# Optimization experiments

Measured on AMD Instinct MI355X. Metric: run time of the kernel, lower is better.

Reference implementation:

```python
import jax, jax.numpy as jnp
import numpy as np

# Config matching init_kwargs: dim=256, input_resolution=(64,64), num_heads=8,
# stride=2, dynamic_factor=2, window_size=8, Attention_Group=2, postype='rel', k=None
DIM, H, W = 256, 64, 64
HEADS, HG, STRIDE, WS, FACTOR = 8, 2, 2, 8, 2.0
GC = DIM // HG                 # channels per attention group (offset net width)
HC = DIM // HEADS              # per-head channels
RH, RW = H // STRIDE, W // STRIDE
WH, WW = H // WS, W // WS
B = 2
MLP_HID = 4 * DIM
EPS = 1e-5


def _grid_sample(img, grid):
    # img: (N, C, H, W); grid: (N, Hg, Wg, 2) with (row, col) in [-1, 1].
    # Bilinear, align_corners=True, zero padding (matches F.grid_sample).
    N, C, Hi, Wi = img.shape
    rows = (grid[..., 0] + 1.0) * 0.5 * (Hi - 1)
    cols = (grid[..., 1] + 1.0) * 0.5 * (Wi - 1)
    r0f = jnp.floor(rows); c0f = jnp.floor(cols)
    wr = rows - r0f; wc = cols - c0f
    r0 = r0f.astype(jnp.int32); c0 = c0f.astype(jnp.int32)

    def gather(ri, ci):
        valid = ((ri >= 0) & (ri < Hi) & (ci >= 0) & (ci < Wi)).astype(img.dtype)
        rc = jnp.clip(ri, 0, Hi - 1); cc = jnp.clip(ci, 0, Wi - 1)
        vals = jax.vmap(lambda im, r, c: im[:, r, c])(img, rc, cc)  # (N, C, Hg, Wg)
        return vals * valid[:, None]

    return (gather(r0, c0) * ((1 - wr) * (1 - wc))[:, None]
            + gather(r0, c0 + 1) * ((1 - wr) * wc)[:, None]
            + gather(r0 + 1, c0) * (wr * (1 - wc))[:, None]
            + gather(r0 + 1, c0 + 1) * (wr * wc)[:, None])


def _ln2d(z, g, b):
    mu = jnp.mean(z, axis=1, keepdims=True)
    var = jnp.var(z, axis=1, keepdims=True)
    return (z - mu) * jax.lax.rsqrt(var + EPS) * g[None, :, None, None] + b[None, :, None, None]


def _conv1x1(z, w, b=None):
    out = jnp.einsum('oc,bchw->bohw', w, z)
    return out if b is None else out + b[None, :, None, None]


def _forward(x, ln1_g, ln1_b, q_w, q_b, k_w, k_b, v_w, v_b,
             off1_w, off2_w, off3_w, bn_g, bn_b, bn_m, bn_v, off4_w,
             posembed, proj_w, proj_b, ln2_g, ln2_b,
             mlp_w1, mlp_b1, mlp_w2, mlp_b2):
    Bx, C = x.shape[0], x.shape[1]
    R, NW, WT = RH * RW, WH * WW, WS * WS
    scale = C ** -0.5  # original uses dim**-0.5 (not head_dim) as default qk scale

    xa = _ln2d(x, ln1_g, ln1_b)
    q = _conv1x1(xa, q_w, q_b)

    # ---- per-group offset prediction: 3 depthwise strided convs -> BN -> GELU -> 1x1 ----
    qg = q.reshape(Bx * HG, GC, H, W)

    def dw(z, w):
        return jax.lax.conv_general_dilated(z, w, (2, 2), ((1, 1), (1, 1)),
                feature_group_count=GC, dimension_numbers=('NCHW', 'OIHW', 'NCHW'))

    o = dw(dw(dw(qg, off1_w), off2_w), off3_w)  # (B*HG, GC, WH, WW)
    o = (o - bn_m[None, :, None, None]) * jax.lax.rsqrt(bn_v + EPS)[None, :, None, None]
    o = o * bn_g[None, :, None, None] + bn_b[None, :, None, None]
    o = jax.nn.gelu(o, approximate=False)
    off = jnp.einsum('oc,bchw->bohw', off4_w, o)               # (B*HG, 2R, WH, WW)
    off = off.reshape(Bx * HG, 2, R, NW).transpose(0, 3, 2, 1)  # (B*HG, NW, R, 2)
    ranges = jnp.array([1.0 / H, 1.0 / W], dtype=x.dtype)
    off = jnp.tanh(off) * ranges * FACTOR

    # ---- reference points normalized to [-1, 1] (align_corners=True convention) ----
    ref_r = (jnp.arange(RH, dtype=x.dtype) * STRIDE) / (H - 1) * 2.0 - 1.0
    ref_c = (jnp.arange(RW, dtype=x.dtype) * STRIDE) / (W - 1) * 2.0 - 1.0
    ref = jnp.stack(jnp.meshgrid(ref_r, ref_c, indexing='ij'), axis=-1).reshape(R, 2)
    grid = off + ref[None, None]                                # (B*HG, NW, R, 2)

    # ---- deformable gather of values at predicted sample locations ----
    value = xa.reshape(Bx * HG, GC, H, W)
    samp = _grid_sample(value, grid).reshape(Bx, C, NW, R)

    kk = _conv1x1(samp, k_w, k_b).reshape(Bx * HEADS, HC, NW, R).transpose(0, 2, 1, 3)
    vv = _conv1x1(samp, v_w, v_b).reshape(Bx * HEADS, HC, NW, R).transpose(0, 2, 1, 3)

    # ---- windowed queries ----
    wq = q.reshape(Bx * HEADS, HC, H, W).transpose(0, 2, 3, 1)
    wq = wq.reshape(Bx * HEADS, WH, WS, WW, WS, HC).transpose(0, 1, 3, 2, 4, 5)
    wq = wq.reshape(Bx * HEADS, NW, WT, HC) * scale

    attn = jnp.einsum('nwqc,nwcr->nwqr', wq, kk)                # (B*h, NW, WT, R)

    # ---- relative position bias: query pixel vs. (stride-spaced) reference point ----
    rel_y = (jnp.arange(RH) * STRIDE)[None, :] - jnp.arange(H)[:, None] + (H - 1)  # (H, RH)
    rel_x = (jnp.arange(RW) * STRIDE)[None, :] - jnp.arange(W)[:, None] + (W - 1)  # (W, RW)
    t = posembed[:, rel_y, :]                                   # (h, H, RH, 2W-1)
    bias = t[:, :, :, rel_x]                                    # (h, H, RH, W, RW)
    bias = bias.transpose(0, 1, 3, 2, 4).reshape(HEADS, H, W, R)
    bias = bias.reshape(HEADS, WH, WS, WW, WS, R).transpose(0, 1, 3, 2, 4, 5)
    bias = bias.reshape(HEADS, NW, WT, R)

    attn = attn.reshape(Bx, HEADS, NW, WT, R) + bias[None]
    attn = jax.nn.softmax(attn, axis=-1).reshape(Bx * HEADS, NW, WT, R)
    out = jnp.einsum('nwqr,nwcr->nwqc', attn, vv)               # (B*h, NW, WT, HC)
    out = out.reshape(Bx * HEADS, WH, WW, WS, WS, HC).transpose(0, 1, 3, 2, 4, 5)
    out = out.reshape(Bx, HEADS, H, W, HC).transpose(0, 1, 4, 2, 3).reshape(Bx, C, H, W)
    out = _conv1x1(out, proj_w, proj_b)

    x = x + out
    xm = _ln2d(x, ln2_g, ln2_b)
    hdn = jax.nn.gelu(_conv1x1(xm, mlp_w1, mlp_b1), approximate=False)
    return x + _conv1x1(hdn, mlp_w2, mlp_b2)


def setup_inputs() -> dict:
    key = jax.random.key(0)
    ks = jax.random.split(key, 16)
    f32 = jnp.float32

    def n(k, shape, std=0.02):
        return jax.random.normal(k, shape, dtype=f32) * std

    R = RH * RW
    return {
        'x': jax.random.normal(ks[0], (B, DIM, H, W), dtype=f32),
        'ln1_g': jnp.ones((DIM,), f32), 'ln1_b': jnp.zeros((DIM,), f32),
        'q_w': n(ks[1], (DIM, DIM)), 'q_b': jnp.zeros((DIM,), f32),
        'k_w': n(ks[2], (DIM, DIM)), 'k_b': jnp.zeros((DIM,), f32),
        'v_w': n(ks[3], (DIM, DIM)), 'v_b': jnp.zeros((DIM,), f32),
        'off1_w': n(ks[4], (GC, 1, 3, 3)),
        'off2_w': n(ks[5], (GC, 1, 3, 3)),
        'off3_w': n(ks[6], (GC, 1, 3, 3)),
        'bn_g': jnp.ones((GC,), f32), 'bn_b': jnp.zeros((GC,), f32),
        'bn_m': jnp.zeros((GC,), f32), 'bn_v': jnp.ones((GC,), f32),
        'off4_w': n(ks[7], (2 * R, GC)),
        'posembed': n(ks[8], (HEADS, 2 * H - 1, 2 * W - 1), std=0.01),
        'proj_w': n(ks[9], (DIM, DIM)), 'proj_b': jnp.zeros((DIM,), f32),
        'ln2_g': jnp.ones((DIM,), f32), 'ln2_b': jnp.zeros((DIM,), f32),
        'mlp_w1': n(ks[10], (MLP_HID, DIM)), 'mlp_b1': jnp.zeros((MLP_HID,), f32),
        'mlp_w2': n(ks[11], (DIM, MLP_HID)), 'mlp_b2': jnp.zeros((DIM,), f32),
    }


def reference(x, ln1_g, ln1_b, q_w, q_b, k_w, k_b, v_w, v_b,
              off1_w, off2_w, off3_w, bn_g, bn_b, bn_m, bn_v, off4_w,
              posembed, proj_w, proj_b, ln2_g, ln2_b,
              mlp_w1, mlp_b1, mlp_w2, mlp_b2):
    return _forward(x, ln1_g, ln1_b, q_w, q_b, k_w, k_b, v_w, v_b,
                    off1_w, off2_w, off3_w, bn_g, bn_b, bn_m, bn_v, off4_w,
                    posembed, proj_w, proj_b, ln2_g, ln2_b,
                    mlp_w1, mlp_b1, mlp_w2, mlp_b2)
```

## Files before the change

### kernel.cpp

```cpp
#include <hip/hip_runtime.h>
#include <hip/hip_bf16.h>
#include <math.h>


typedef __hip_bfloat16 bf16;
typedef __bf16 bf16x8 __attribute__((ext_vector_type(8)));
typedef float f32x4 __attribute__((ext_vector_type(4)));

union U16x8 { uint4 u4; unsigned short us[8]; };

__device__ __forceinline__ float cvt(float x) { return x; }
__device__ __forceinline__ float cvt(bf16 x) { return __bfloat162float(x); }
__device__ __forceinline__ float b2f(unsigned short u) {
  union { float f; unsigned int v; } x; x.v = ((unsigned int)u) << 16; return x.f;
}
__device__ __forceinline__ unsigned short f2b(float f) {
  bf16 h = __float2bfloat16(f);
  return *reinterpret_cast<unsigned short*>(&h);
}
__device__ __forceinline__ float gelu_f(float x) {
  return 0.5f * x * (1.0f + erff(x * 0.7071067811865475f));
}
__device__ __forceinline__ void stout(float* p, float v) { *p = v; }
__device__ __forceinline__ void stout(bf16* p, float v) { *p = __float2bfloat16(v); }

__global__ __launch_bounds__(256) void ln1_kernel(
    const float* __restrict__ x, const float* __restrict__ g,
    const float* __restrict__ bta, bf16* __restrict__ out,
    float* __restrict__ xnhwc)
{
  __shared__ float s1[8][32], s2[8][32];
  __shared__ unsigned short tb[32][264];
  int t = threadIdx.x;
  int pos = t & 31, cs = t >> 5;
  int p = blockIdx.x * 32 + pos;
  int bb = p >> 12, hw = p & 4095;
  const float* xp = x + (size_t)bb * 256 * 4096 + hw;
  float vloc[32];
  float sum = 0.f, ss = 0.f;
#pragma unroll
  for (int i = 0; i < 32; ++i) {
    float v = xp[(size_t)(cs * 32 + i) * 4096];
    vloc[i] = v; sum += v; ss += v * v;
  }
  s1[cs][pos] = sum; s2[cs][pos] = ss;
  {
    float* xo = xnhwc + (size_t)p * 256 + cs * 32;
#pragma unroll
    for (int qd = 0; qd < 8; ++qd)
      *(float4*)(xo + qd * 4) = make_float4(vloc[qd*4], vloc[qd*4+1],
                                            vloc[qd*4+2], vloc[qd*4+3]);
  }
  __syncthreads();
  if (cs == 0) {
    float S = 0.f, Q = 0.f;
#pragma unroll
    for (int i = 0; i < 8; ++i) { S += s1[i][pos]; Q += s2[i][pos]; }
    float mu = S * (1.f / 256.f);
    float var = Q * (1.f / 256.f) - mu * mu;
    s1[0][pos] = mu;
    s2[0][pos] = rsqrtf(var + 1e-5f);
  }
  __syncthreads();
  float mu = s1[0][pos], rs = s2[0][pos];
#pragma unroll
  for (int i = 0; i < 32; ++i) {
    int c = cs * 32 + i;
    tb[pos][c] = f2b((vloc[i] - mu) * rs * g[c] + bta[c]);
  }
  __syncthreads();
  int px = t >> 3, grp = t & 7;
  bf16* op = out + ((size_t)blockIdx.x * 32 + px) * 256 + grp * 32;
#pragma unroll
  for (int q = 0; q < 4; ++q)
    *(uint4*)(op + q * 8) = *(const uint4*)&tb[px][grp * 32 + q * 8];
}

__global__ __launch_bounds__(256) void ln2_kernel(
    const bf16* __restrict__ xin, const float* __restrict__ g,
    const float* __restrict__ bta, bf16* __restrict__ out)
{
  __shared__ float sa[8][32], sb[8][32];
  __shared__ float mu_s[32], rs_s[32];
  int t = threadIdx.x;
  int px = t >> 3, grp = t & 7;
  size_t p = (size_t)blockIdx.x * 32 + px;
  const bf16* xp = xin + p * 256 + grp * 32;
  float v[32]; float sum = 0.f, ss = 0.f;
#pragma unroll
  for (int q = 0; q < 4; ++q) {
    U16x8 u; u.u4 = *(const uint4*)(xp + q * 8);
#pragma unroll
    for (int j = 0; j < 8; ++j) {
      float f = b2f(u.us[j]); v[q * 8 + j] = f; sum += f; ss += f * f;
    }
  }
  sa[grp][px] = sum; sb[grp][px] = ss;
  __syncthreads();
  if (t < 32) {
    float S = 0.f, Q = 0.f;
#pragma unroll
    for (int i = 0; i < 8; ++i) { S += sa[i][t]; Q += sb[i][t]; }
    float mu = S * (1.f / 256.f);
    mu_s[t] = mu;
    rs_s[t] = rsqrtf(Q * (1.f / 256.f) - mu * mu + 1e-5f);
  }
  __syncthreads();
  float mu = mu_s[px], rs = rs_s[px];
  bf16* op = out + p * 256 + grp * 32;
#pragma unroll
  for (int q = 0; q < 4; ++q) {
    U16x8 o;
#pragma unroll
    for (int j = 0; j < 8; ++j) {
      int c = grp * 32 + q * 8 + j;
      o.us[j] = f2b((v[q * 8 + j] - mu) * rs * g[c] + bta[c]);
    }
    *(uint4*)(op + q * 8) = o.u4;
  }
}

template<int OUTM, int RESM, int ACT>
__global__ __launch_bounds__(256) void mgemm_kernel(
    const bf16* __restrict__ A, const float* __restrict__ Bw,
    const float* __restrict__ bias, const void* __restrict__ res,
    void* __restrict__ out, int N, int K, int lda, int ldb)
{
  constexpr int AB_BYTES = (128 * 72 + 64 * 72) * 2;
  constexpr int T_BYTES  = 64 * 133 * 4;
  constexpr int SH_BYTES = (OUTM == 1 && T_BYTES > AB_BYTES) ? T_BYTES : AB_BYTES;
  __shared__ __attribute__((aligned(16))) char shraw[SH_BYTES];
  auto As = reinterpret_cast<unsigned short(*)[72]>(shraw);
  auto Bs = reinterpret_cast<unsigned short(*)[72]>(shraw + 128 * 72 * 2);
  float (*T)[133] = reinterpret_cast<float(*)[133]>(shraw);

  int t = threadIdx.x;
  int m0 = blockIdx.y * 128, n0 = blockIdx.x * 64;
  int lane = t & 63, w = t >> 6;
  int l15 = lane & 15, quad = lane >> 4;
  int wm = (w >> 1) * 64, wn = (w & 1) * 32;
  f32x4 acc[4][2];
#pragma unroll
  for (int mt = 0; mt < 4; ++mt)
#pragma unroll
    for (int nt = 0; nt < 2; ++nt) acc[mt][nt] = (f32x4){0.f, 0.f, 0.f, 0.f};

  for (int k0 = 0; k0 < K; k0 += 64) {
#pragma unroll
    for (int i = 0; i < 4; ++i) {
      int idx = t + i * 256;
      int m = idx >> 3, oc = (idx & 7) * 8;
      *(uint4*)&As[m][oc] = *(const uint4*)(A + (size_t)(m0 + m) * lda + k0 + oc);
    }
    {
      int n = t >> 2, h = (t & 3) * 16;
      const float* bp = Bw + (size_t)(n0 + n) * ldb + k0 + h;
      float4 f0 = *(const float4*)(bp);
      float4 f1 = *(const float4*)(bp + 4);
      float4 f2 = *(const float4*)(bp + 8);
      float4 f3 = *(const float4*)(bp + 12);
      U16x8 u0, u1;
      u0.us[0] = f2b(f0.x); u0.us[1] = f2b(f0.y); u0.us[2] = f2b(f0.z); u0.us[3] = f2b(f0.w);
      u0.us[4] = f2b(f1.x); u0.us[5] = f2b(f1.y); u0.us[6] = f2b(f1.z); u0.us[7] = f2b(f1.w);
      u1.us[0] = f2b(f2.x); u1.us[1] = f2b(f2.y); u1.us[2] = f2b(f2.z); u1.us[3] = f2b(f2.w);
      u1.us[4] = f2b(f3.x); u1.us[5] = f2b(f3.y); u1.us[6] = f2b(f3.z); u1.us[7] = f2b(f3.w);
      *(uint4*)&Bs[n][h] = u0.u4;
      *(uint4*)&Bs[n][h + 8] = u1.u4;
    }
    __syncthreads();
#pragma unroll
    for (int ks = 0; ks < 2; ++ks) {
      bf16x8 af[4], bfr[2];
#pragma unroll
      for (int mt = 0; mt < 4; ++mt)
        af[mt] = __builtin_bit_cast(bf16x8,
            *(const uint4*)&As[wm + mt * 16 + l15][ks * 32 + quad * 8]);
#pragma unroll
      for (int nt = 0; nt < 2; ++nt)
        bfr[nt] = __builtin_bit_cast(bf16x8,
            *(const uint4*)&Bs[wn + nt * 16 + l15][ks * 32 + quad * 8]);
#pragma unroll
      for (int mt = 0; mt < 4; ++mt)
#pragma unroll
        for (int nt = 0; nt < 2; ++nt)
          acc[mt][nt] = __builtin_amdgcn_mfma_f32_16x16x32_bf16(
              af[mt], bfr[nt], acc[mt][nt], 0, 0, 0);
    }
    __syncthreads();
  }
  float bv[2];
#pragma unroll
  for (int nt = 0; nt < 2; ++nt)
    bv[nt] = bias ? bias[n0 + wn + nt * 16 + l15] : 0.f;
#pragma unroll
  for (int mt = 0; mt < 4; ++mt) {
#pragma unroll
    for (int nt = 0; nt < 2; ++nt) {
#pragma unroll
      for (int reg = 0; reg < 4; ++reg) {
        int m = m0 + wm + mt * 16 + quad * 4 + reg;
        int n = n0 + wn + nt * 16 + l15;
        float v = acc[mt][nt][reg] + bv[nt];
        if constexpr (ACT == 1) v = gelu_f(v);
        if constexpr (RESM == 1)
          v += ((const float*)res)[(size_t)m * N + n];
        if constexpr (RESM == 2)
          v += b2f(((const unsigned short*)res)[(size_t)m * N + n]);
        if constexpr (OUTM == 0)
          ((unsigned short*)out)[(size_t)m * N + n] = f2b(v);
        if constexpr (OUTM == 1)
          T[(n - n0)][(m - m0)] = v;
        if constexpr (OUTM == 3) {
          float val = tanhf(v) * (2.0f / 64.0f);
          int coord = n >> 10, r = n & 1023;
          int rc = coord ? (r & 31) : (r >> 5);
          float ref = rc * (4.0f / 63.0f) - 1.0f;
          float pix = (val + ref + 1.0f) * 31.5f;
          float* dst = coord ? (float*)res : (float*)out;
          dst[(size_t)m * 1024 + r] = pix;
        }
      }
    }
  }
  if constexpr (OUTM == 1) {
    __syncthreads();
    int nl = t >> 2, seg = t & 3;
    int bI = m0 >> 12, hw0 = m0 & 4095;
    float* op = (float*)out + ((size_t)bI * 256 + n0 + nl) * 4096 + hw0 + seg * 32;
#pragma unroll
    for (int k = 0; k < 32; ++k) op[k] = T[nl][seg * 32 + k];
  }
}

template<typename TI, typename TO, int IC>
__global__ __launch_bounds__(256) void dwconv_kernel(
    const TI* __restrict__ in, const float* __restrict__ wgt,
    TO* __restrict__ out, int Hi, int Wi, int Ho, int Wo, int fuse,
    const float* __restrict__ bg_, const float* __restrict__ bb_,
    const float* __restrict__ bm_, const float* __restrict__ bv_)
{
  int idx = blockIdx.x * 256 + threadIdx.x;
  int c = idx & 127;
  int pp = idx >> 7;
  int ow = pp % Wo, oh = (pp / Wo) % Ho, bgi = pp / (Wo * Ho);
  const TI* ip;
  if constexpr (IC == 256)
    ip = in + ((size_t)(bgi >> 1) * 4096) * 256 + (bgi & 1) * 128 + c;
  else
    ip = in + ((size_t)bgi * Hi * Wi) * 128 + c;
  float acc = 0.f;
#pragma unroll
  for (int ky = 0; ky < 3; ++ky) {
    int ih = oh * 2 - 1 + ky;
    if ((unsigned)ih >= (unsigned)Hi) continue;
#pragma unroll
    for (int kx = 0; kx < 3; ++kx) {
      int iw = ow * 2 - 1 + kx;
      if ((unsigned)iw >= (unsigned)Wi) continue;
      acc += wgt[c * 9 + ky * 3 + kx] * cvt(ip[(size_t)(ih * Wi + iw) * IC]);
    }
  }
  if (fuse) {
    acc = (acc - bm_[c]) * rsqrtf(bv_[c] + 1e-5f) * bg_[c] + bb_[c];
    acc = gelu_f(acc);
  }
  stout(out + idx, acc);
}

__device__ __forceinline__ void gather_issue(
    int rc0, int b, int nw, int gr_r, int choff,
    const float* __restrict__ rows_, const float* __restrict__ cols_,
    const unsigned short* __restrict__ Kimg, const unsigned short* __restrict__ Vimg,
    uint4* kc, uint4* vc, float* wgt)
{
#pragma unroll
  for (int g = 0; g < 2; ++g) {
    size_t cbase = ((size_t)(b * 2 + g) * 64 + nw) * 1024 + rc0 + gr_r;
    float rowf = rows_[cbase];
    float colf = cols_[cbase];
    float r0f = floorf(rowf), c0f = floorf(colf);
    float wr = rowf - r0f, wc = colf - c0f;
    int r0 = (int)r0f, c0 = (int)c0f;
    bool rv0 = ((unsigned)r0 < 64u), rv1 = ((unsigned)(r0 + 1) < 64u);
    bool cv0 = ((unsigned)c0 < 64u), cv1 = ((unsigned)(c0 + 1) < 64u);
    wgt[g * 4 + 0] = (rv0 && cv0) ? (1.f - wr) * (1.f - wc) : 0.f;
    wgt[g * 4 + 1] = (rv0 && cv1) ? (1.f - wr) * wc : 0.f;
    wgt[g * 4 + 2] = (rv1 && cv0) ? wr * (1.f - wc) : 0.f;
    wgt[g * 4 + 3] = (rv1 && cv1) ? wr * wc : 0.f;
    int ra = min(max(r0, 0), 63), rb2 = min(max(r0 + 1, 0), 63);
    int ca = min(max(c0, 0), 63), cb2 = min(max(c0 + 1, 0), 63);
    size_t pb = ((size_t)g * 8192 + (size_t)b * 4096) * 256 + choff;
    size_t o00 = pb + (size_t)(ra * 64 + ca) * 256;
    size_t o01 = pb + (size_t)(ra * 64 + cb2) * 256;
    size_t o10 = pb + (size_t)(rb2 * 64 + ca) * 256;
    size_t o11 = pb + (size_t)(rb2 * 64 + cb2) * 256;
    kc[g * 4 + 0] = *(const uint4*)(Kimg + o00); vc[g * 4 + 0] = *(const uint4*)(Vimg + o00);
    kc[g * 4 + 1] = *(const uint4*)(Kimg + o01); vc[g * 4 + 1] = *(const uint4*)(Vimg + o01);
    kc[g * 4 + 2] = *(const uint4*)(Kimg + o10); vc[g * 4 + 2] = *(const uint4*)(Vimg + o10);
    kc[g * 4 + 3] = *(const uint4*)(Kimg + o11); vc[g * 4 + 3] = *(const uint4*)(Vimg + o11);
  }
}

__global__ __launch_bounds__(256) void attn_kernel(
    const bf16* __restrict__ qbuf, const unsigned short* __restrict__ Kimg,
    const unsigned short* __restrict__ Vimg, const float* __restrict__ rows_,
    const float* __restrict__ cols_, const float* __restrict__ vbv,
    const float* __restrict__ pe, bf16* __restrict__ aout)
{
  __shared__ unsigned short ks[2][64][40];
  __shared__ unsigned short vs[2][32][80];
  __shared__ unsigned short PsQs[64][72];
  __shared__ unsigned short pesb[70][72];

  int blk = blockIdx.x;
  int b = blk & 1, head = (blk >> 1) & 7, nw = blk >> 4;
  int wh = nw >> 3, ww = nw & 7;
  int t = threadIdx.x;
  int lane = t & 63, w = t >> 6;
  int l15 = lane & 15, quad = lane >> 4;
  int qc0 = head * 32;
  int gr_r = t >> 2, gr_seg = t & 3;
  int choff = qc0 + gr_seg * 8;

  {
    int qt = t >> 2, oct = t & 3;
    int h = wh * 8 + (qt >> 3), wcol = ww * 8 + (qt & 7);
    const bf16* src = qbuf + ((size_t)b * 4096 + h * 64 + wcol) * 256 + qc0 + oct * 8;
    U16x8 u; u.u4 = *(const uint4*)src;
    U16x8 o;
#pragma unroll
    for (int j = 0; j < 8; ++j) o.us[j] = f2b(b2f(u.us[j]) * 0.0625f);
    *(uint4*)&PsQs[qt][oct * 8] = o.u4;
  }
  int ry0 = 56 - wh * 8, rx0 = 56 - ww * 8;
  for (int i = t; i < 70 * 70; i += 256) {
    int yy = i / 70, xx = i % 70;
    pesb[yy][xx] = f2b(pe[(size_t)head * 16129 + (ry0 + yy) * 127 + rx0 + xx]);
  }

  uint4 kc[8], vc[8];
  float wgt[8];
  gather_issue(0, b, nw, gr_r, choff, rows_, cols_, Kimg, Vimg, kc, vc, wgt);
  {
    float aK[8] = {0,0,0,0,0,0,0,0}, aV[8] = {0,0,0,0,0,0,0,0};
#pragma unroll
    for (int gc = 0; gc < 8; ++gc) {
      U16x8 ku, vu; ku.u4 = kc[gc]; vu.u4 = vc[gc];
      float wv = wgt[gc];
#pragma unroll
      for (int j = 0; j < 8; ++j) { aK[j] += wv * b2f(ku.us[j]); aV[j] += wv * b2f(vu.us[j]); }
    }
    U16x8 ok;
#pragma unroll
    for (int j = 0; j < 8; ++j) ok.us[j] = f2b(aK[j]);
    *(uint4*)&ks[0][gr_r][gr_seg * 8] = ok.u4;
#pragma unroll
    for (int j = 0; j < 8; ++j) vs[0][gr_seg * 8 + j][gr_r] = f2b(aV[j]);
  }
  __syncthreads();

  bf16x8 aQ;
  {
    uint4 u = *(const uint4*)&PsQs[w * 16 + l15][quad * 8];
    aQ = __builtin_bit_cast(bf16x8, u);
  }
  float m[4] = {-1e30f, -1e30f, -1e30f, -1e30f};
  float l[4] = {0.f, 0.f, 0.f, 0.f};
  f32x4 oacc[2];
  oacc[0] = (f32x4){0.f, 0.f, 0.f, 0.f};
  oacc[1] = (f32x4){0.f, 0.f, 0.f, 0.f};

  for (int c = 0; c < 16; ++c) {
    if (c) __syncthreads();
    int cur = c & 1, rc0 = c * 64;
    if (c < 15)
      gather_issue(rc0 + 64, b, nw, gr_r, choff, rows_, cols_, Kimg, Vimg, kc, vc, wgt);

    f32x4 s[4];
#pragma unroll
    for (int nt = 0; nt < 4; ++nt) {
      uint4 u = *(const uint4*)&ks[cur][nt * 16 + l15][quad * 8];
      bf16x8 bK = __builtin_bit_cast(bf16x8, u);
      f32x4 z = (f32x4){0.f, 0.f, 0.f, 0.f};
      s[nt] = __builtin_amdgcn_mfma_f32_16x16x32_bf16(aQ, bK, z, 0, 0, 0);
    }
#pragma unroll
    for (int nt = 0; nt < 4; ++nt) {
      int rg_ = nt * 16 + l15;
      int rrow = (rc0 + rg_) >> 5, rcol = rg_ & 31;
#pragma unroll
      for (int reg = 0; reg < 4; ++reg) {
        int q = w * 16 + quad * 4 + reg;
        s[nt][reg] += b2f(pesb[2 * rrow + 7 - (q >> 3)][2 * rcol + 7 - (q & 7)]);
      }
    }
    float alpha[4];
#pragma unroll
    for (int reg = 0; reg < 4; ++reg) {
      float mx = fmaxf(fmaxf(s[0][reg], s[1][reg]), fmaxf(s[2][reg], s[3][reg]));
      mx = fmaxf(mx, __shfl_xor(mx, 1, 64));
      mx = fmaxf(mx, __shfl_xor(mx, 2, 64));
      mx = fmaxf(mx, __shfl_xor(mx, 4, 64));
      mx = fmaxf(mx, __shfl_xor(mx, 8, 64));
      float mn = fmaxf(m[reg], mx);
      alpha[reg] = __expf(m[reg] - mn);
      m[reg] = mn;
      float ps = 0.f;
#pragma unroll
      for (int nt = 0; nt < 4; ++nt) {
        float p = __expf(s[nt][reg] - mn);
        PsQs[w * 16 + quad * 4 + reg][nt * 16 + l15] = f2b(p);
        ps += p;
      }
      ps += __shfl_xor(ps, 1, 64);
      ps += __shfl_xor(ps, 2, 64);
      ps += __shfl_xor(ps, 4, 64);
      ps += __shfl_xor(ps, 8, 64);
      l[reg] = l[reg] * alpha[reg] + ps;
      oacc[0][reg] *= alpha[reg];
      oacc[1][reg] *= alpha[reg];
    }
#pragma unroll
    for (int kst = 0; kst < 2; ++kst) {
      uint4 up = *(const uint4*)&PsQs[w * 16 + l15][kst * 32 + quad * 8];
      bf16x8 pA = __builtin_bit_cast(bf16x8, up);
#pragma unroll
      for (int nt2 = 0; nt2 < 2; ++nt2) {
        uint4 uv = *(const uint4*)&vs[cur][nt2 * 16 + l15][kst * 32 + quad * 8];
        bf16x8 vB = __builtin_bit_cast(bf16x8, uv);
        oacc[nt2] = __builtin_amdgcn_mfma_f32_16x16x32_bf16(pA, vB, oacc[nt2], 0, 0, 0);
      }
    }
    if (c < 15) {
      float aK[8] = {0,0,0,0,0,0,0,0}, aV[8] = {0,0,0,0,0,0,0,0};
#pragma unroll
      for (int gc = 0; gc < 8; ++gc) {
        U16x8 ku, vu; ku.u4 = kc[gc]; vu.u4 = vc[gc];
        float wv = wgt[gc];
#pragma unroll
        for (int j = 0; j < 8; ++j) { aK[j] += wv * b2f(ku.us[j]); aV[j] += wv * b2f(vu.us[j]); }
      }
      int nxt = cur ^ 1;
      U16x8 ok;
#pragma unroll
      for (int j = 0; j < 8; ++j) ok.us[j] = f2b(aK[j]);
      *(uint4*)&ks[nxt][gr_r][gr_seg * 8] = ok.u4;
#pragma unroll
      for (int j = 0; j < 8; ++j) vs[nxt][gr_seg * 8 + j][gr_r] = f2b(aV[j]);
    }
  }
#pragma unroll
  for (int nt2 = 0; nt2 < 2; ++nt2) {
    float vbias = vbv[qc0 + nt2 * 16 + l15];
#pragma unroll
    for (int reg = 0; reg < 4; ++reg) {
      int q = w * 16 + quad * 4 + reg;
      size_t p = (size_t)b * 4096 + (wh * 8 + (q >> 3)) * 64 + ww * 8 + (q & 7);
      aout[p * 256 + qc0 + nt2 * 16 + l15] =
          __float2bfloat16(oacc[nt2][reg] / l[reg] + vbias);
    }
  }
}

extern "C" void kernel_launch(void* const* d_in, const int* in_sizes, int n_in,
                              void* d_out, int out_size, void* d_ws, size_t ws_size,
                              hipStream_t stream) {
  (void)in_sizes; (void)n_in; (void)out_size; (void)ws_size;
  const float* x     = (const float*)d_in[0];
  const float* ln1g  = (const float*)d_in[1];
  const float* ln1b  = (const float*)d_in[2];
  const float* q_w   = (const float*)d_in[3];
  const float* q_b   = (const float*)d_in[4];
  const float* k_w   = (const float*)d_in[5];
  const float* k_b   = (const float*)d_in[6];
  const float* v_w   = (const float*)d_in[7];
  const float* v_b   = (const float*)d_in[8];
  const float* off1w = (const float*)d_in[9];
  const float* off2w = (const float*)d_in[10];
  const float* off3w = (const float*)d_in[11];
  const float* bng   = (const float*)d_in[12];
  const float* bnb   = (const float*)d_in[13];
  const float* bnm   = (const float*)d_in[14];
  const float* bnv   = (const float*)d_in[15];
  const float* off4w = (const float*)d_in[16];
  const float* pe    = (const float*)d_in[17];
  const float* pjw   = (const float*)d_in[18];
  const float* pjb   = (const float*)d_in[19];
  const float* ln2g  = (const float*)d_in[20];
  const float* ln2b  = (const float*)d_in[21];
  const float* w1    = (const float*)d_in[22];
  const float* b1    = (const float*)d_in[23];
  const float* w2    = (const float*)d_in[24];
  const float* b2    = (const float*)d_in[25];
  (void)k_b;
  float* outp = (float*)d_out;

  char* W = (char*)d_ws;
  bf16*  xa    = (bf16*) (W + 0);
  bf16*  qb    = (bf16*) (W + 4194304);
  float* dw1   = (float*)(W + 8388608);
  float* dw2   = (float*)(W + 10485760);
  bf16*  dw3b  = (bf16*) (W + 11010048);
  float* rows  = (float*)(W + 11141120);
  float* cols  = (float*)(W + 12189696);
  bf16*  Kimg  = (bf16*) (W + 13238272);
  bf16*  Vimg  = (bf16*) (W + 21626880);
  bf16*  x2    = (bf16*) (W + 30015488);
  float* xnhwc = (float*)(W + 34209792);
  bf16*  aout = xa;
  bf16*  xm   = qb;
  bf16*  hdn  = Kimg;

  ln1_kernel<<<256, 256, 0, stream>>>(x, ln1g, ln1b, xa, xnhwc);
  mgemm_kernel<0, 0, 0><<<dim3(4, 64), 256, 0, stream>>>(
      xa, q_w, q_b, nullptr, qb, 256, 256, 256, 256);
  dwconv_kernel<bf16, float, 256><<<2048, 256, 0, stream>>>(
      qb, off1w, dw1, 64, 64, 32, 32, 0, nullptr, nullptr, nullptr, nullptr);
  dwconv_kernel<float, float, 128><<<512, 256, 0, stream>>>(
      dw1, off2w, dw2, 32, 32, 16, 16, 0, nullptr, nullptr, nullptr, nullptr);
  dwconv_kernel<float, bf16, 128><<<128, 256, 0, stream>>>(
      dw2, off3w, dw3b, 16, 16, 8, 8, 1, bng, bnb, bnm, bnv);
  mgemm_kernel<3, 0, 0><<<dim3(32, 2), 256, 0, stream>>>(
      dw3b, off4w, nullptr, (const void*)cols, rows, 2048, 128, 128, 128);
  mgemm_kernel<0, 0, 0><<<dim3(4, 64), 256, 0, stream>>>(
      xa,       k_w,       nullptr, nullptr, Kimg,           256, 128, 256, 256);
  mgemm_kernel<0, 0, 0><<<dim3(4, 64), 256, 0, stream>>>(
      xa + 128, k_w + 128, nullptr, nullptr, Kimg + 2097152, 256, 128, 256, 256);
  mgemm_kernel<0, 0, 0><<<dim3(4, 64), 256, 0, stream>>>(
      xa,       v_w,       nullptr, nullptr, Vimg,           256, 128, 256, 256);
  mgemm_kernel<0, 0, 0><<<dim3(4, 64), 256, 0, stream>>>(
      xa + 128, v_w + 128, nullptr, nullptr, Vimg + 2097152, 256, 128, 256, 256);
  attn_kernel<<<1024, 256, 0, stream>>>(
      qb, (const unsigned short*)Kimg, (const unsigned short*)Vimg,
      rows, cols, v_b, pe, aout);
  mgemm_kernel<0, 1, 0><<<dim3(4, 64), 256, 0, stream>>>(
      aout, pjw, pjb, (const void*)xnhwc, x2, 256, 256, 256, 256);
  ln2_kernel<<<256, 256, 0, stream>>>(x2, ln2g, ln2b, xm);
  mgemm_kernel<0, 0, 1><<<dim3(16, 64), 256, 0, stream>>>(
      xm, w1, b1, nullptr, hdn, 1024, 256, 256, 256);
  mgemm_kernel<1, 2, 0><<<dim3(4, 64), 256, 0, stream>>>(
      hdn, w2, b2, (const void*)x2, outp, 256, 1024, 1024, 1024);
}
```

Before: 319.0 us.

## Pre-convert weights to bf16, fuse QKV GEMMs, add BM template, swizzle V smem

A prep kernel converts all GEMM weights to bf16 once per call, so each GEMM block no longer converts fp32 weights while loading tiles. The Q, K and V projections become one GEMM against a concatenated, zero-padded weight matrix with a new scatter output mode, replacing five launches. Small-N GEMMs use a 64-row tile to launch more blocks. The attention V tile in shared memory uses an XOR swizzle instead of padding to avoid bank conflicts. In exchange it adds an extra launch and weight traffic each call, and the zero-padded K/V halves double the MACs for those projections.

```diff
diff --git a/kernel.cpp b/kernel.cpp
--- a/kernel.cpp
+++ b/kernel.cpp
@@ -23,6 +23,45 @@
 }
 __device__ __forceinline__ void stout(float* p, float v) { *p = v; }
 __device__ __forceinline__ void stout(bf16* p, float v) { *p = __float2bfloat16(v); }
+
+__global__ __launch_bounds__(256) void prep_kernel(
+    const float* __restrict__ q_w, const float* __restrict__ q_b,
+    const float* __restrict__ k_w, const float* __restrict__ v_w,
+    const float* __restrict__ pjw, const float* __restrict__ w1,
+    const float* __restrict__ w2, const float* __restrict__ off4w,
+    unsigned short* __restrict__ wqkv, float* __restrict__ bqkv,
+    unsigned short* __restrict__ wproj, unsigned short* __restrict__ wmlp1,
+    unsigned short* __restrict__ wmlp2, unsigned short* __restrict__ woff4)
+{
+  int idx = blockIdx.x * 256 + threadIdx.x;
+  const int S0 = 1280 * 256;
+  const int S1 = S0 + 1280;
+  const int S2 = S1 + 256 * 256;
+  const int S3 = S2 + 1024 * 256;
+  const int S4 = S3 + 256 * 1024;
+  const int S5 = S4 + 2048 * 128;
+  if (idx < S0) {
+    int n = idx >> 8, c = idx & 255;
+    float v;
+    if (n < 256)       v = q_w[n * 256 + c];
+    else if (n < 512)  v = (c < 128)  ? k_w[(n - 256) * 256 + c] : 0.f;
+    else if (n < 768)  v = (c >= 128) ? k_w[(n - 512) * 256 + c] : 0.f;
+    else if (n < 1024) v = (c < 128)  ? v_w[(n - 768) * 256 + c] : 0.f;
+    else               v = (c >= 128) ? v_w[(n - 1024) * 256 + c] : 0.f;
+    wqkv[idx] = f2b(v);
+  } else if (idx < S1) {
+    int n = idx - S0;
+    bqkv[n] = (n < 256) ? q_b[n] : 0.f;
+  } else if (idx < S2) {
+    wproj[idx - S1] = f2b(pjw[idx - S1]);
+  } else if (idx < S3) {
+    wmlp1[idx - S2] = f2b(w1[idx - S2]);
+  } else if (idx < S4) {
+    wmlp2[idx - S3] = f2b(w2[idx - S3]);
+  } else if (idx < S5) {
+    woff4[idx - S4] = f2b(off4w[idx - S4]);
+  }
+}
 
 __global__ __launch_bounds__(256) void ln1_kernel(
     const float* __restrict__ x, const float* __restrict__ g,
@@ -120,59 +159,52 @@
   }
 }
 
-template<int OUTM, int RESM, int ACT>
+template<int OUTM, int RESM, int ACT, int BM>
 __global__ __launch_bounds__(256) void mgemm_kernel(
-    const bf16* __restrict__ A, const float* __restrict__ Bw,
+    const bf16* __restrict__ A, const unsigned short* __restrict__ Bw,
     const float* __restrict__ bias, const void* __restrict__ res,
     void* __restrict__ out, int N, int K, int lda, int ldb)
 {
-  constexpr int AB_BYTES = (128 * 72 + 64 * 72) * 2;
-  constexpr int T_BYTES  = 64 * 133 * 4;
+  constexpr int MT = BM / 32;
+  constexpr int AB_BYTES = (BM + 64) * 72 * 2;
+  constexpr int T_LD = BM + 5;
+  constexpr int T_BYTES = 64 * T_LD * 4;
   constexpr int SH_BYTES = (OUTM == 1 && T_BYTES > AB_BYTES) ? T_BYTES : AB_BYTES;
   __shared__ __attribute__((aligned(16))) char shraw[SH_BYTES];
   auto As = reinterpret_cast<unsigned short(*)[72]>(shraw);
-  auto Bs = reinterpret_cast<unsigned short(*)[72]>(shraw + 128 * 72 * 2);
-  float (*T)[133] = reinterpret_cast<float(*)[133]>(shraw);
+  auto Bs = reinterpret_cast<unsigned short(*)[72]>(shraw + BM * 72 * 2);
+  float (*T)[T_LD] = reinterpret_cast<float(*)[T_LD]>(shraw);
 
   int t = threadIdx.x;
-  int m0 = blockIdx.y * 128, n0 = blockIdx.x * 64;
+  int m0 = blockIdx.y * BM, n0 = blockIdx.x * 64;
   int lane = t & 63, w = t >> 6;
   int l15 = lane & 15, quad = lane >> 4;
-  int wm = (w >> 1) * 64, wn = (w & 1) * 32;
-  f32x4 acc[4][2];
-#pragma unroll
-  for (int mt = 0; mt < 4; ++mt)
+  int wm = (w >> 1) * (BM / 2), wn = (w & 1) * 32;
+  f32x4 acc[MT][2];
+#pragma unroll
+  for (int mt = 0; mt < MT; ++mt)
 #pragma unroll
     for (int nt = 0; nt < 2; ++nt) acc[mt][nt] = (f32x4){0.f, 0.f, 0.f, 0.f};
 
   for (int k0 = 0; k0 < K; k0 += 64) {
 #pragma unroll
-    for (int i = 0; i < 4; ++i) {
+    for (int i = 0; i < MT; ++i) {
       int idx = t + i * 256;
       int m = idx >> 3, oc = (idx & 7) * 8;
       *(uint4*)&As[m][oc] = *(const uint4*)(A + (size_t)(m0 + m) * lda + k0 + oc);
     }
-    {
-      int n = t >> 2, h = (t & 3) * 16;
-      const float* bp = Bw + (size_t)(n0 + n) * ldb + k0 + h;
-      float4 f0 = *(const float4*)(bp);
-      float4 f1 = *(const float4*)(bp + 4);
-      float4 f2 = *(const float4*)(bp + 8);
-      float4 f3 = *(const float4*)(bp + 12);
-      U16x8 u0, u1;
-      u0.us[0] = f2b(f0.x); u0.us[1] = f2b(f0.y); u0.us[2] = f2b(f0.z); u0.us[3] = f2b(f0.w);
-      u0.us[4] = f2b(f1.x); u0.us[5] = f2b(f1.y); u0.us[6] = f2b(f1.z); u0.us[7] = f2b(f1.w);
-      u1.us[0] = f2b(f2.x); u1.us[1] = f2b(f2.y); u1.us[2] = f2b(f2.z); u1.us[3] = f2b(f2.w);
-      u1.us[4] = f2b(f3.x); u1.us[5] = f2b(f3.y); u1.us[6] = f2b(f3.z); u1.us[7] = f2b(f3.w);
-      *(uint4*)&Bs[n][h] = u0.u4;
-      *(uint4*)&Bs[n][h + 8] = u1.u4;
+#pragma unroll
+    for (int i = 0; i < 2; ++i) {
+      int idx = t + i * 256;
+      int n = idx >> 3, oc = (idx & 7) * 8;
+      *(uint4*)&Bs[n][oc] = *(const uint4*)(Bw + (size_t)(n0 + n) * ldb + k0 + oc);
     }
     __syncthreads();
 #pragma unroll
     for (int ks = 0; ks < 2; ++ks) {
-      bf16x8 af[4], bfr[2];
-#pragma unroll
-      for (int mt = 0; mt < 4; ++mt)
+      bf16x8 af[MT], bfr[2];
+#pragma unroll
+      for (int mt = 0; mt < MT; ++mt)
         af[mt] = __builtin_bit_cast(bf16x8,
             *(const uint4*)&As[wm + mt * 16 + l15][ks * 32 + quad * 8]);
 #pragma unroll
@@ -180,7 +212,7 @@
         bfr[nt] = __builtin_bit_cast(bf16x8,
             *(const uint4*)&Bs[wn + nt * 16 + l15][ks * 32 + quad * 8]);
 #pragma unroll
-      for (int mt = 0; mt < 4; ++mt)
+      for (int mt = 0; mt < MT; ++mt)
 #pragma unroll
         for (int nt = 0; nt < 2; ++nt)
           acc[mt][nt] = __builtin_amdgcn_mfma_f32_16x16x32_bf16(
@@ -193,7 +225,7 @@
   for (int nt = 0; nt < 2; ++nt)
     bv[nt] = bias ? bias[n0 + wn + nt * 16 + l15] : 0.f;
 #pragma unroll
-  for (int mt = 0; mt < 4; ++mt) {
+  for (int mt = 0; mt < MT; ++mt) {
 #pragma unroll
     for (int nt = 0; nt < 2; ++nt) {
 #pragma unroll
@@ -219,16 +251,22 @@
           float* dst = coord ? (float*)res : (float*)out;
           dst[(size_t)m * 1024 + r] = pix;
         }
+        if constexpr (OUTM == 4)
+          ((unsigned short*)out)[((size_t)(n >> 8) * 8192 + m) * 256 + (n & 255)] = f2b(v);
       }
     }
   }
   if constexpr (OUTM == 1) {
     __syncthreads();
-    int nl = t >> 2, seg = t & 3;
-    int bI = m0 >> 12, hw0 = m0 & 4095;
-    float* op = (float*)out + ((size_t)bI * 256 + n0 + nl) * 4096 + hw0 + seg * 32;
-#pragma unroll
-    for (int k = 0; k < 32; ++k) op[k] = T[nl][seg * 32 + k];
+    constexpr int SEGS = BM / 32;
+    int units = 64 * SEGS;
+    if (t < units) {
+      int nl = t / SEGS, seg = t % SEGS;
+      int bI = m0 >> 12, hw0 = m0 & 4095;
+      float* op = (float*)out + ((size_t)bI * 256 + n0 + nl) * 4096 + hw0 + seg * 32;
+#pragma unroll
+      for (int k = 0; k < 32; ++k) op[k] = T[nl][seg * 32 + k];
+    }
   }
 }
 
@@ -308,7 +346,7 @@
     const float* __restrict__ pe, bf16* __restrict__ aout)
 {
   __shared__ unsigned short ks[2][64][40];
-  __shared__ unsigned short vs[2][32][80];
+  __shared__ unsigned short vs[2][32][72];
   __shared__ unsigned short PsQs[64][72];
   __shared__ unsigned short pesb[70][72];
 
@@ -355,7 +393,10 @@
     for (int j = 0; j < 8; ++j) ok.us[j] = f2b(aK[j]);
     *(uint4*)&ks[0][gr_r][gr_seg * 8] = ok.u4;
 #pragma unroll
-    for (int j = 0; j < 8; ++j) vs[0][gr_seg * 8 + j][gr_r] = f2b(aV[j]);
+    for (int j = 0; j < 8; ++j) {
+      int row = gr_seg * 8 + j;
+      vs[0][row][gr_r ^ (((row >> 3) & 1) * 8)] = f2b(aV[j]);
+    }
   }
   __syncthreads();
 
@@ -426,7 +467,9 @@
       bf16x8 pA = __builtin_bit_cast(bf16x8, up);
 #pragma unroll
       for (int nt2 = 0; nt2 < 2; ++nt2) {
-        uint4 uv = *(const uint4*)&vs[cur][nt2 * 16 + l15][kst * 32 + quad * 8];
+        int row = nt2 * 16 + l15;
+        int cbase = (kst * 32 + quad * 8) ^ (((row >> 3) & 1) * 8);
+        uint4 uv = *(const uint4*)&vs[cur][row][cbase];
         bf16x8 vB = __builtin_bit_cast(bf16x8, uv);
         oacc[nt2] = __builtin_amdgcn_mfma_f32_16x16x32_bf16(pA, vB, oacc[nt2], 0, 0, 0);
       }
@@ -446,7 +489,10 @@
       for (int j = 0; j < 8; ++j) ok.us[j] = f2b(aK[j]);
       *(uint4*)&ks[nxt][gr_r][gr_seg * 8] = ok.u4;
 #pragma unroll
-      for (int j = 0; j < 8; ++j) vs[nxt][gr_seg * 8 + j][gr_r] = f2b(aV[j]);
+      for (int j = 0; j < 8; ++j) {
+        int row = gr_seg * 8 + j;
+        vs[nxt][row][gr_r ^ (((row >> 3) & 1) * 8)] = f2b(aV[j]);
+      }
     }
   }
 #pragma unroll
@@ -497,47 +543,48 @@
 
   char* W = (char*)d_ws;
   bf16*  xa    = (bf16*) (W + 0);
-  bf16*  qb    = (bf16*) (W + 4194304);
   float* dw1   = (float*)(W + 8388608);
   float* dw2   = (float*)(W + 10485760);
   bf16*  dw3b  = (bf16*) (W + 11010048);
   float* rows  = (float*)(W + 11141120);
   float* cols  = (float*)(W + 12189696);
-  bf16*  Kimg  = (bf16*) (W + 13238272);
-  bf16*  Vimg  = (bf16*) (W + 21626880);
-  bf16*  x2    = (bf16*) (W + 30015488);
-  float* xnhwc = (float*)(W + 34209792);
+  bf16*  qkv   = (bf16*) (W + 13238272);
+  bf16*  qb    = qkv;
+  bf16*  Kimg  = qkv + 2097152;
+  bf16*  Vimg  = qkv + 3 * 2097152;
+  bf16*  x2    = (bf16*) (W + 34209792);
+  float* xnhwc = (float*)(W + 38404096);
+  unsigned short* wqkv  = (unsigned short*)(W + 46792704);
+  float*          bqkv  = (float*)         (W + 47448064);
+  unsigned short* wproj = (unsigned short*)(W + 47453184);
+  unsigned short* wmlp1 = (unsigned short*)(W + 47584256);
+  unsigned short* wmlp2 = (unsigned short*)(W + 48108544);
+  unsigned short* woff4 = (unsigned short*)(W + 48632832);
   bf16*  aout = xa;
-  bf16*  xm   = qb;
+  bf16*  xm   = xa;
   bf16*  hdn  = Kimg;
 
+  prep_kernel<<<4613, 256, 0, stream>>>(q_w, q_b, k_w, v_w, pjw, w1, w2, off4w,
+                                        wqkv, bqkv, wproj, wmlp1, wmlp2, woff4);
   ln1_kernel<<<256, 256, 0, stream>>>(x, ln1g, ln1b, xa, xnhwc);
-  mgemm_kernel<0, 0, 0><<<dim3(4, 64), 256, 0, stream>>>(
-      xa, q_w, q_b, nullptr, qb, 256, 256, 256, 256);
+  mgemm_kernel<4, 0, 0, 128><<<dim3(20, 64), 256, 0, stream>>>(
+      xa, wqkv, bqkv, nullptr, qkv, 1280, 256, 256, 256);
   dwconv_kernel<bf16, float, 256><<<2048, 256, 0, stream>>>(
       qb, off1w, dw1, 64, 64, 32, 32, 0, nullptr, nullptr, nullptr, nullptr);
   dwconv_kernel<float, float, 128><<<512, 256, 0, stream>>>(
       dw1, off2w, dw2, 32, 32, 16, 16, 0, nullptr, nullptr, nullptr, nullptr);
   dwconv_kernel<float, bf16, 128><<<128, 256, 0, stream>>>(
       dw2, off3w, dw3b, 16, 16, 8, 8, 1, bng, bnb, bnm, bnv);
-  mgemm_kernel<3, 0, 0><<<dim3(32, 2), 256, 0, stream>>>(
-      dw3b, off4w, nullptr, (const void*)cols, rows, 2048, 128, 128, 128);
-  mgemm_kernel<0, 0, 0><<<dim3(4, 64), 256, 0, stream>>>(
-      xa,       k_w,       nullptr, nullptr, Kimg,           256, 128, 256, 256);
-  mgemm_kernel<0, 0, 0><<<dim3(4, 64), 256, 0, stream>>>(
-      xa + 128, k_w + 128, nullptr, nullptr, Kimg + 2097152, 256, 128, 256, 256);
-  mgemm_kernel<0, 0, 0><<<dim3(4, 64), 256, 0, stream>>>(
-      xa,       v_w,       nullptr, nullptr, Vimg,           256, 128, 256, 256);
-  mgemm_kernel<0, 0, 0><<<dim3(4, 64), 256, 0, stream>>>(
-      xa + 128, v_w + 128, nullptr, nullptr, Vimg + 2097152, 256, 128, 256, 256);
+  mgemm_kernel<3, 0, 0, 128><<<dim3(32, 2), 256, 0, stream>>>(
+      dw3b, woff4, nullptr, (const void*)cols, rows, 2048, 128, 128, 128);
   attn_kernel<<<1024, 256, 0, stream>>>(
       qb, (const unsigned short*)Kimg, (const unsigned short*)Vimg,
       rows, cols, v_b, pe, aout);
-  mgemm_kernel<0, 1, 0><<<dim3(4, 64), 256, 0, stream>>>(
-      aout, pjw, pjb, (const void*)xnhwc, x2, 256, 256, 256, 256);
+  mgemm_kernel<0, 1, 0, 64><<<dim3(4, 128), 256, 0, stream>>>(
+      aout, wproj, pjb, (const void*)xnhwc, x2, 256, 256, 256, 256);
   ln2_kernel<<<256, 256, 0, stream>>>(x2, ln2g, ln2b, xm);
-  mgemm_kernel<0, 0, 1><<<dim3(16, 64), 256, 0, stream>>>(
-      xm, w1, b1, nullptr, hdn, 1024, 256, 256, 256);
-  mgemm_kernel<1, 2, 0><<<dim3(4, 64), 256, 0, stream>>>(
-      hdn, w2, b2, (const void*)x2, outp, 256, 1024, 1024, 1024);
-}
+  mgemm_kernel<0, 0, 1, 128><<<dim3(16, 64), 256, 0, stream>>>(
+      xm, wmlp1, b1, nullptr, hdn, 1024, 256, 256, 256);
+  mgemm_kernel<1, 2, 0, 64><<<dim3(4, 128), 256, 0, stream>>>(
+      hdn, wmlp2, b2, (const void*)x2, outp, 256, 1024, 1024, 1024);
+}
```

New measurement: 320.9 us. About the same (+0.6%).
